# Performance work log

Measured on AMD Instinct MI355X. Metric: run time of the kernel, lower is better.

Reference implementation:

```python
import jax, jax.numpy as jnp
import numpy as np

N_REC = 12288  # 12 * nside^2, nside=32


def _mlp(x, w1, b1, w2, b2):
    # two-layer MLP with SiLU, as in GraphCast-style edge embedders
    return jnp.dot(jax.nn.silu(jnp.dot(x, w1) + b1), w2) + b2


def setup_inputs() -> dict:
    key = jax.random.key(0)
    ks = jax.random.split(key, 12)
    B, E, D_X, D_EDGE = 2, 393216, 128, 4
    EDGE_IN, EDGE_OUT, LIN_OUT = D_EDGE + D_X, 256, 256

    def glorot(k, shape):
        fan = shape[0] + shape[1]
        return jax.random.normal(k, shape, jnp.float32) * jnp.sqrt(2.0 / fan)

    return {
        "x": jax.random.normal(ks[0], (B, E, D_X), jnp.float32),
        "edge_attr": jax.random.normal(ks[1], (E, D_EDGE), jnp.float32),
        "edge_index": jax.random.randint(ks[2], (2, E), 0, N_REC, jnp.int64),
        "w1e": glorot(ks[3], (EDGE_IN, EDGE_OUT)),
        "b1e": jnp.zeros((EDGE_OUT,), jnp.float32),
        "w2e": glorot(ks[4], (EDGE_OUT, EDGE_OUT)),
        "b2e": jnp.zeros((EDGE_OUT,), jnp.float32),
        "w1f": glorot(ks[5], (EDGE_OUT, LIN_OUT)),
        "b1f": jnp.zeros((LIN_OUT,), jnp.float32),
        "w2f": glorot(ks[6], (LIN_OUT, LIN_OUT)),
        "b2f": jnp.zeros((LIN_OUT,), jnp.float32),
    }


def reference(x, edge_attr, edge_index, w1e, b1e, w2e, b2e, w1f, b1f, w2f, b2f):
    B = x.shape[0]
    # broadcast edge_attr over batch and concat with per-edge grid features
    ea = jnp.broadcast_to(edge_attr[None], (B,) + edge_attr.shape)  # [B,E,d_edge]
    v_g_prime = jnp.concatenate([ea, x], axis=-1)                    # [B,E,edge_in]
    v_g = _mlp(v_g_prime, w1e, b1e, w2e, b2e)                        # [B,E,edge_out]
    # scatter-sum edges into receiver nodes (edge_index[1]) along dim 1
    recv = edge_index[1]
    v_m_sum = jnp.zeros((B, N_REC, v_g.shape[-1]), v_g.dtype).at[:, recv].add(v_g)
    return _mlp(v_m_sum, w1f, b1f, w2f, b2f)                         # [B,N_REC,lin_out]
```

## Files before the change

### kernel.cpp

```cpp
#include <hip/hip_runtime.h>
#include <hip/hip_bf16.h>

#define E_EDGES 393216
#define NRECV   12288
#define DX      128
#define BATCH   2

typedef short bf16x8 __attribute__((ext_vector_type(8)));
typedef float f32x4  __attribute__((ext_vector_type(4)));

__device__ __forceinline__ unsigned short f2bf(float f) {
  union { float f; unsigned u; } v; v.f = f;
  unsigned r = v.u + 0x7FFFu + ((v.u >> 16) & 1u);
  return (unsigned short)(r >> 16);
}

__device__ __forceinline__ unsigned pk2(float a, float b) {
  __hip_bfloat162 h = __float22bfloat162_rn(make_float2(a, b));
  union { __hip_bfloat162 h; unsigned u; } c; c.h = h;
  return c.u;
}

__device__ __forceinline__ float silu_f(float v) {
  float e = __builtin_amdgcn_exp2f(v * -1.44269504089f);
  return v * __builtin_amdgcn_rcpf(1.0f + e);
}

__global__ __launch_bounds__(256) void zero_kernel(float4* __restrict__ p, int n4) {
  int i = blockIdx.x * 256 + threadIdx.x;
  int stride = gridDim.x * 256;
  float4 z = make_float4(0.f, 0.f, 0.f, 0.f);
  for (; i < n4; i += stride) p[i] = z;
}

__global__ __launch_bounds__(256) void swz_all_kernel(
    const float* __restrict__ w1e, const float* __restrict__ b1e,
    const float* __restrict__ w2e, const float* __restrict__ w1f,
    const float* __restrict__ w2f,
    unsigned short* __restrict__ w1sw, unsigned short* __restrict__ w2esw,
    unsigned short* __restrict__ w1fsw, unsigned short* __restrict__ w2fsw) {
  int blk = blockIdx.x;
  if (blk < 160) {
    int t = blk * 256 + threadIdx.x;
    int j = t & 7, l = (t >> 3) & 63, rest = t >> 9;
    int nf = rest & 15, ks = rest >> 4;
    int k = ks * 32 + (l >> 4) * 8 + j;
    int n = nf * 16 + (l & 15);
    float v = (k < 132) ? w1e[k * 256 + n] : (k == 132 ? b1e[n] : 0.0f);
    w1sw[t] = f2bf(v);
  } else {
    int g = blk - 160;
    int which = g >> 8;
    int t = (g & 255) * 256 + threadIdx.x;
    const float* W = (which == 0) ? w2e : (which == 1) ? w1f : w2f;
    unsigned short* O = (which == 0) ? w2esw : (which == 1) ? w1fsw : w2fsw;
    int j = t & 7, l = (t >> 3) & 63, rest = t >> 9;
    int nf = rest & 15, ks = rest >> 4;
    int k = ks * 32 + (l >> 4) * 8 + j;
    int n = nf * 16 + (l & 15);
    O[t] = f2bf(W[k * 256 + n]);
  }
}

__global__ void hist_kernel(const int* __restrict__ recv, int* __restrict__ cnt) {
  int e = blockIdx.x * 256 + threadIdx.x;
  if (e < E_EDGES) atomicAdd(&cnt[recv[e]], 1);
}

__global__ __launch_bounds__(256) void scan_kernel(const int* __restrict__ cnt,
                                                   int* __restrict__ head) {
  __shared__ int ts[256];
  const int t = threadIdx.x;
  const int base = t * 48;
  int s = 0;
#pragma unroll
  for (int i = 0; i < 48; ++i) s += cnt[base + i];
  ts[t] = s;
  __syncthreads();
  for (int d = 1; d < 256; d <<= 1) {
    int v = (t >= d) ? ts[t - d] : 0;
    __syncthreads();
    ts[t] += v;
    __syncthreads();
  }
  int run = (t == 0) ? 0 : ts[t - 1];
  for (int i = 0; i < 48; ++i) { head[base + i] = run; run += cnt[base + i]; }
}

__global__ void scatter_kernel(const int* __restrict__ recv, int* __restrict__ head,
                               int* __restrict__ perm) {
  int e = blockIdx.x * 256 + threadIdx.x;
  if (e < E_EDGES) {
    int pos = atomicAdd(&head[recv[e]], 1);
    perm[pos] = e;
  }
}

__global__ __launch_bounds__(256, 4) void edge_kernel(
    const float* __restrict__ x, const float* __restrict__ edge_attr,
    const int* __restrict__ recv, const int* __restrict__ perm,
    const unsigned short* __restrict__ w1sw, float* __restrict__ s) {
  __shared__ __align__(16) char As[64 * 384];
  __shared__ int rs[64];
  __shared__ int seg_recv[64];
  __shared__ unsigned seg32[16];

  const int tid = threadIdx.x;
  const int l  = tid & 63;
  const int w  = tid >> 6;
  const int lo = l & 15, hi = l >> 4;
  const int p0 = blockIdx.x * 64;
  const int b  = blockIdx.y;

  const int r = tid >> 2, q = tid & 3;
  const int er = perm[p0 + r];
  const float4* xr = (const float4*)(x + ((size_t)b * E_EDGES + er) * DX);
  float4 xv[8];
#pragma unroll
  for (int i = 0; i < 8; ++i) xv[i] = xr[i * 4 + q];

  float4 ea;
  if (tid < 64) {
    int e1 = perm[p0 + tid];
    rs[tid] = recv[e1];
    ea = *(const float4*)(edge_attr + (size_t)e1 * 4);
  }

  for (int idx = tid; idx < 960; idx += 256) {
    int rr = idx / 15, k2 = idx - rr * 15;
    int byte0 = 264 + 8 * k2;
    uint2 vz = make_uint2(k2 == 0 ? 0x00003F80u : 0u, 0u);
    *(uint2*)(As + rr * 384 + (byte0 ^ ((rr & 7) << 4))) = vz;
  }

  {
    const int rx = (r & 7) << 4;
#pragma unroll
    for (int i = 0; i < 8; ++i) {
      int t = i * 4 + q;
      int byte0 = 8 + 8 * t;
      *(uint2*)(As + r * 384 + (byte0 ^ rx)) =
          make_uint2(pk2(xv[i].x, xv[i].y), pk2(xv[i].z, xv[i].w));
    }
  }
  if (tid < 64) {
    *(uint2*)(As + tid * 384 + ((tid & 7) << 4)) =
        make_uint2(pk2(ea.x, ea.y), pk2(ea.z, ea.w));
  }
  __syncthreads();

  const int flag = (l == 63) || (rs[l + 1] != rs[l]);
  const unsigned long long segmask = __ballot(flag);
  const int nseg = __popcll(segmask);
  if (tid < 64) {
    int sid = __popcll(segmask & ((1ull << tid) - 1ull));
    ((unsigned char*)seg32)[tid] = (unsigned char)sid;
    if (flag) seg_recv[sid] = rs[tid];
  }

  f32x4 acc[4][4] = {};
  const int axor = (lo & 7) << 4;
#pragma unroll
  for (int kk = 0; kk < 5; ++kk) {
    bf16x8 a[4], bb[4];
#pragma unroll
    for (int mf = 0; mf < 4; ++mf)
      a[mf] = *(const bf16x8*)(As + (mf * 16 + lo) * 384 + ((kk * 64 + hi * 16) ^ axor));
#pragma unroll
    for (int nf = 0; nf < 4; ++nf)
      bb[nf] = *(const bf16x8*)&w1sw[(size_t)(((kk * 16) + (w * 4 + nf)) * 64 + l) * 8];
#pragma unroll
    for (int mf = 0; mf < 4; ++mf)
#pragma unroll
      for (int nf = 0; nf < 4; ++nf)
        acc[mf][nf] = __builtin_amdgcn_mfma_f32_16x16x32_bf16(a[mf], bb[nf], acc[mf][nf], 0, 0, 0);
  }
  __syncthreads();

  unsigned pkd[4][4][2];
#pragma unroll
  for (int mf = 0; mf < 4; ++mf)
#pragma unroll
    for (int nf = 0; nf < 4; ++nf) {
      float v0 = silu_f(acc[mf][nf][0]);
      float v1 = silu_f(acc[mf][nf][1]);
      float v2 = silu_f(acc[mf][nf][2]);
      float v3 = silu_f(acc[mf][nf][3]);
      pkd[mf][nf][0] = pk2(v0, v1);
      pkd[mf][nf][1] = pk2(v2, v3);
    }

  unsigned hbw[2][4][4];
#pragma unroll
  for (int kk = 0; kk < 2; ++kk)
#pragma unroll
    for (int nf = 0; nf < 4; ++nf)
#pragma unroll
      for (int t = 0; t < 4; ++t) {
        int src = ((hi & 1) * 2 + (t >> 1)) * 16 + lo;
        int a0 = __shfl((int)pkd[2 * kk][nf][t & 1], src, 64);
        int a1 = __shfl((int)pkd[2 * kk + 1][nf][t & 1], src, 64);
        hbw[kk][nf][t] = (hi & 2) ? (unsigned)a1 : (unsigned)a0;
      }

  float* sb = s + (size_t)b * NRECV * 256;
  for (int p = 0; p * 16 < nseg; ++p) {
    union { unsigned u[4]; bf16x8 v; } ia[2];
#pragma unroll
    for (int kk = 0; kk < 2; ++kk) {
      unsigned d0 = seg32[kk * 8 + hi * 2];
      unsigned d1 = seg32[kk * 8 + hi * 2 + 1];
      unsigned tgt = (unsigned)(lo + p * 16);
      ia[kk].u[0] = (((d0 & 255u) == tgt) ? 0x3F80u : 0u) |
                    ((((d0 >> 8) & 255u) == tgt) ? 0x3F800000u : 0u);
      ia[kk].u[1] = ((((d0 >> 16) & 255u) == tgt) ? 0x3F80u : 0u) |
                    (((d0 >> 24) == tgt) ? 0x3F800000u : 0u);
      ia[kk].u[2] = (((d1 & 255u) == tgt) ? 0x3F80u : 0u) |
                    ((((d1 >> 8) & 255u) == tgt) ? 0x3F800000u : 0u);
      ia[kk].u[3] = ((((d1 >> 16) & 255u) == tgt) ? 0x3F80u : 0u) |
                    (((d1 >> 24) == tgt) ? 0x3F800000u : 0u);
    }
    f32x4 accS[4] = {};
#pragma unroll
    for (int kk = 0; kk < 2; ++kk)
#pragma unroll
      for (int nf = 0; nf < 4; ++nf) {
        union { unsigned u[4]; bf16x8 v; } hb;
        hb.u[0] = hbw[kk][nf][0]; hb.u[1] = hbw[kk][nf][1];
        hb.u[2] = hbw[kk][nf][2]; hb.u[3] = hbw[kk][nf][3];
        accS[nf] = __builtin_amdgcn_mfma_f32_16x16x32_bf16(ia[kk].v, hb.v, accS[nf], 0, 0, 0);
      }
#pragma unroll
    for (int j = 0; j < 4; ++j) {
      int sidx = p * 16 + hi * 4 + j;
      if (sidx < nseg) {
        int rcv = seg_recv[sidx];
#pragma unroll
        for (int nf = 0; nf < 4; ++nf)
          atomicAdd(sb + (size_t)rcv * 256 + w * 64 + nf * 16 + lo, accS[nf][j]);
      }
    }
  }
}

__device__ __forceinline__ void gemm64(const unsigned short* Ns,
                                       const unsigned short* __restrict__ Bsw,
                                       int w, int l, f32x4 acc[4][4]) {
  const int lo = l & 15, hi = l >> 4;
#pragma unroll
  for (int kk = 0; kk < 8; ++kk) {
    bf16x8 a[4], bb[4];
#pragma unroll
    for (int mf = 0; mf < 4; ++mf)
      a[mf] = *(const bf16x8*)&Ns[(mf * 16 + lo) * 264 + kk * 32 + hi * 8];
#pragma unroll
    for (int nf = 0; nf < 4; ++nf)
      bb[nf] = *(const bf16x8*)&Bsw[(size_t)(((kk * 16) + (w * 4 + nf)) * 64 + l) * 8];
#pragma unroll
    for (int mf = 0; mf < 4; ++mf)
#pragma unroll
      for (int nf = 0; nf < 4; ++nf)
        acc[mf][nf] = __builtin_amdgcn_mfma_f32_16x16x32_bf16(a[mf], bb[nf], acc[mf][nf], 0, 0, 0);
  }
}

__global__ __launch_bounds__(256) void node_kernel(
    const float* __restrict__ s, const int* __restrict__ cnt,
    const unsigned short* __restrict__ w2esw, const float* __restrict__ b2e,
    const unsigned short* __restrict__ w1fsw, const float* __restrict__ b1f,
    const unsigned short* __restrict__ w2fsw, const float* __restrict__ b2f,
    float* __restrict__ out) {
  __shared__ unsigned short Ns[64 * 264];
  __shared__ int   cntl[64];
  __shared__ float bias1[256], bias2[256], bias3[256];

  const int tid = threadIdx.x;
  const int l  = tid & 63;
  const int w  = tid >> 6;
  const int lo = l & 15, hi = l >> 4;
  const int r0 = blockIdx.x * 64;
  const int b  = blockIdx.y;

  const float4* sb = (const float4*)(s + ((size_t)b * NRECV + r0) * 256);
#pragma unroll
  for (int i = 0; i < 16; ++i) {
    int f = i * 256 + tid;
    float4 v = sb[f];
    int g = f * 4;
    int row = g >> 8, col = g & 255;
    *(uint2*)&Ns[row * 264 + col] = make_uint2(pk2(v.x, v.y), pk2(v.z, v.w));
  }
  if (tid < 64) cntl[tid] = cnt[r0 + tid];
  bias1[tid] = b2e[tid];
  bias2[tid] = b1f[tid];
  bias3[tid] = b2f[tid];
  __syncthreads();

  {
    f32x4 acc[4][4] = {};
    gemm64(Ns, w2esw, w, l, acc);
    __syncthreads();
#pragma unroll
    for (int mf = 0; mf < 4; ++mf)
#pragma unroll
      for (int nf = 0; nf < 4; ++nf) {
        const int col = w * 64 + nf * 16 + lo;
#pragma unroll
        for (int j = 0; j < 4; ++j) {
          const int row = mf * 16 + hi * 4 + j;
          float v = acc[mf][nf][j] + (float)cntl[row] * bias1[col];
          Ns[row * 264 + col] = f2bf(v);
        }
      }
    __syncthreads();
  }
  {
    f32x4 acc[4][4] = {};
    gemm64(Ns, w1fsw, w, l, acc);
    __syncthreads();
#pragma unroll
    for (int mf = 0; mf < 4; ++mf)
#pragma unroll
      for (int nf = 0; nf < 4; ++nf) {
        const int col = w * 64 + nf * 16 + lo;
#pragma unroll
        for (int j = 0; j < 4; ++j) {
          const int row = mf * 16 + hi * 4 + j;
          float v = silu_f(acc[mf][nf][j] + bias2[col]);
          Ns[row * 264 + col] = f2bf(v);
        }
      }
    __syncthreads();
  }
  {
    f32x4 acc[4][4] = {};
    gemm64(Ns, w2fsw, w, l, acc);
#pragma unroll
    for (int mf = 0; mf < 4; ++mf)
#pragma unroll
      for (int nf = 0; nf < 4; ++nf) {
        const int col = w * 64 + nf * 16 + lo;
#pragma unroll
        for (int j = 0; j < 4; ++j) {
          const int row = mf * 16 + hi * 4 + j;
          out[((size_t)b * NRECV + r0 + row) * 256 + col] = acc[mf][nf][j] + bias3[col];
        }
      }
  }
}

extern "C" void kernel_launch(void* const* d_in, const int* in_sizes, int n_in,
                              void* d_out, int out_size, void* d_ws, size_t ws_size,
                              hipStream_t stream) {
  const float* x         = (const float*)d_in[0];
  const float* edge_attr = (const float*)d_in[1];
  const int*   edge_idx  = (const int*)d_in[2];
  const float* w1e       = (const float*)d_in[3];
  const float* b1e       = (const float*)d_in[4];
  const float* w2e       = (const float*)d_in[5];
  const float* b2e       = (const float*)d_in[6];
  const float* w1f       = (const float*)d_in[7];
  const float* b1f       = (const float*)d_in[8];
  const float* w2f       = (const float*)d_in[9];
  const float* b2f       = (const float*)d_in[10];
  float* out = (float*)d_out;

  char* ws = (char*)d_ws;
  float*          sbuf  = (float*)(ws + 0);
  int*            cnt   = (int*)(ws + 25165824);
  int*            head  = (int*)(ws + 25214976);
  int*            perm  = (int*)(ws + 25264128);
  unsigned short* w1sw  = (unsigned short*)(ws + 26836992);
  unsigned short* w2esw = (unsigned short*)(ws + 26918912);
  unsigned short* w1fsw = (unsigned short*)(ws + 27049984);
  unsigned short* w2fsw = (unsigned short*)(ws + 27181056);

  zero_kernel<<<2048, 256, 0, stream>>>((float4*)ws, 1575936);

  swz_all_kernel<<<928, 256, 0, stream>>>(w1e, b1e, w2e, w1f, w2f,
                                          w1sw, w2esw, w1fsw, w2fsw);

  const int* recv = edge_idx + E_EDGES;
  hist_kernel<<<E_EDGES / 256, 256, 0, stream>>>(recv, cnt);
  scan_kernel<<<1, 256, 0, stream>>>(cnt, head);
  scatter_kernel<<<E_EDGES / 256, 256, 0, stream>>>(recv, head, perm);

  dim3 eg(E_EDGES / 64, BATCH);
  edge_kernel<<<eg, 256, 0, stream>>>(x, edge_attr, recv, perm, w1sw, sbuf);

  dim3 ng(NRECV / 64, BATCH);
  node_kernel<<<ng, 256, 0, stream>>>(sbuf, cnt, w2esw, b2e, w1fsw, b1f, w2fsw, b2f, out);
}
```

Before: 250.3 us.

## Make edge kernel persistent over eight tiles with register double-buffered prefetch

Each edge_kernel block now handles 8 consecutive 64-edge tiles instead of one. While the current tile runs its GEMM and segment-reduce, the next tile's x rows, edge_attr and receiver ids are prefetched into a second register set. The zero padding of the shared A tile is written once per block rather than once per tile. The aim is to hide gather latency behind MFMA work and cut per-block launch overhead, at the cost of more registers, fewer blocks (768×2) and possibly lower occupancy.

```diff
diff --git a/kernel.cpp b/kernel.cpp
--- a/kernel.cpp
+++ b/kernel.cpp
@@ -5,6 +5,7 @@
 #define NRECV   12288
 #define DX      128
 #define BATCH   2
+#define NT      8
 
 typedef short bf16x8 __attribute__((ext_vector_type(8)));
 typedef float f32x4  __attribute__((ext_vector_type(4)));
@@ -109,22 +110,12 @@
   const int l  = tid & 63;
   const int w  = tid >> 6;
   const int lo = l & 15, hi = l >> 4;
-  const int p0 = blockIdx.x * 64;
+  const int tile0 = blockIdx.x * NT;
   const int b  = blockIdx.y;
-
   const int r = tid >> 2, q = tid & 3;
-  const int er = perm[p0 + r];
-  const float4* xr = (const float4*)(x + ((size_t)b * E_EDGES + er) * DX);
-  float4 xv[8];
-#pragma unroll
-  for (int i = 0; i < 8; ++i) xv[i] = xr[i * 4 + q];
-
-  float4 ea;
-  if (tid < 64) {
-    int e1 = perm[p0 + tid];
-    rs[tid] = recv[e1];
-    ea = *(const float4*)(edge_attr + (size_t)e1 * 4);
-  }
+  const int rx = (r & 7) << 4;
+  const int axor = (lo & 7) << 4;
+  float* const sb = s + (size_t)b * NRECV * 256;
 
   for (int idx = tid; idx < 960; idx += 256) {
     int rr = idx / 15, k2 = idx - rr * 15;
@@ -133,113 +124,140 @@
     *(uint2*)(As + rr * 384 + (byte0 ^ ((rr & 7) << 4))) = vz;
   }
 
+  float4 xvA[8], xvB[8];
+  float4 eaA = make_float4(0, 0, 0, 0), eaB = make_float4(0, 0, 0, 0);
+  int rsA = 0, rsB = 0;
+
   {
-    const int rx = (r & 7) << 4;
+    const int p0 = tile0 * 64;
+    const int er = perm[p0 + r];
+    const float4* xr = (const float4*)(x + ((size_t)b * E_EDGES + er) * DX);
+#pragma unroll
+    for (int i = 0; i < 8; ++i) xvA[i] = xr[i * 4 + q];
+    if (tid < 64) {
+      int e1 = perm[p0 + tid];
+      rsA = recv[e1];
+      eaA = *(const float4*)(edge_attr + (size_t)e1 * 4);
+    }
+  }
+
+  auto body = [&](int t, float4 (&xvC)[8], float4& eaC, int& rsC,
+                  float4 (&xvN)[8], float4& eaN, int& rsN) {
 #pragma unroll
     for (int i = 0; i < 8; ++i) {
-      int t = i * 4 + q;
-      int byte0 = 8 + 8 * t;
+      int t_ = i * 4 + q;
+      int byte0 = 8 + 8 * t_;
       *(uint2*)(As + r * 384 + (byte0 ^ rx)) =
-          make_uint2(pk2(xv[i].x, xv[i].y), pk2(xv[i].z, xv[i].w));
-    }
-  }
-  if (tid < 64) {
-    *(uint2*)(As + tid * 384 + ((tid & 7) << 4)) =
-        make_uint2(pk2(ea.x, ea.y), pk2(ea.z, ea.w));
-  }
-  __syncthreads();
-
-  const int flag = (l == 63) || (rs[l + 1] != rs[l]);
-  const unsigned long long segmask = __ballot(flag);
-  const int nseg = __popcll(segmask);
-  if (tid < 64) {
-    int sid = __popcll(segmask & ((1ull << tid) - 1ull));
-    ((unsigned char*)seg32)[tid] = (unsigned char)sid;
-    if (flag) seg_recv[sid] = rs[tid];
-  }
-
-  f32x4 acc[4][4] = {};
-  const int axor = (lo & 7) << 4;
-#pragma unroll
-  for (int kk = 0; kk < 5; ++kk) {
-    bf16x8 a[4], bb[4];
-#pragma unroll
-    for (int mf = 0; mf < 4; ++mf)
-      a[mf] = *(const bf16x8*)(As + (mf * 16 + lo) * 384 + ((kk * 64 + hi * 16) ^ axor));
-#pragma unroll
-    for (int nf = 0; nf < 4; ++nf)
-      bb[nf] = *(const bf16x8*)&w1sw[(size_t)(((kk * 16) + (w * 4 + nf)) * 64 + l) * 8];
-#pragma unroll
-    for (int mf = 0; mf < 4; ++mf)
-#pragma unroll
-      for (int nf = 0; nf < 4; ++nf)
-        acc[mf][nf] = __builtin_amdgcn_mfma_f32_16x16x32_bf16(a[mf], bb[nf], acc[mf][nf], 0, 0, 0);
-  }
-  __syncthreads();
-
-  unsigned pkd[4][4][2];
-#pragma unroll
-  for (int mf = 0; mf < 4; ++mf)
-#pragma unroll
-    for (int nf = 0; nf < 4; ++nf) {
-      float v0 = silu_f(acc[mf][nf][0]);
-      float v1 = silu_f(acc[mf][nf][1]);
-      float v2 = silu_f(acc[mf][nf][2]);
-      float v3 = silu_f(acc[mf][nf][3]);
-      pkd[mf][nf][0] = pk2(v0, v1);
-      pkd[mf][nf][1] = pk2(v2, v3);
-    }
-
-  unsigned hbw[2][4][4];
-#pragma unroll
-  for (int kk = 0; kk < 2; ++kk)
-#pragma unroll
-    for (int nf = 0; nf < 4; ++nf)
-#pragma unroll
-      for (int t = 0; t < 4; ++t) {
-        int src = ((hi & 1) * 2 + (t >> 1)) * 16 + lo;
-        int a0 = __shfl((int)pkd[2 * kk][nf][t & 1], src, 64);
-        int a1 = __shfl((int)pkd[2 * kk + 1][nf][t & 1], src, 64);
-        hbw[kk][nf][t] = (hi & 2) ? (unsigned)a1 : (unsigned)a0;
-      }
-
-  float* sb = s + (size_t)b * NRECV * 256;
-  for (int p = 0; p * 16 < nseg; ++p) {
-    union { unsigned u[4]; bf16x8 v; } ia[2];
-#pragma unroll
-    for (int kk = 0; kk < 2; ++kk) {
-      unsigned d0 = seg32[kk * 8 + hi * 2];
-      unsigned d1 = seg32[kk * 8 + hi * 2 + 1];
-      unsigned tgt = (unsigned)(lo + p * 16);
-      ia[kk].u[0] = (((d0 & 255u) == tgt) ? 0x3F80u : 0u) |
-                    ((((d0 >> 8) & 255u) == tgt) ? 0x3F800000u : 0u);
-      ia[kk].u[1] = ((((d0 >> 16) & 255u) == tgt) ? 0x3F80u : 0u) |
-                    (((d0 >> 24) == tgt) ? 0x3F800000u : 0u);
-      ia[kk].u[2] = (((d1 & 255u) == tgt) ? 0x3F80u : 0u) |
-                    ((((d1 >> 8) & 255u) == tgt) ? 0x3F800000u : 0u);
-      ia[kk].u[3] = ((((d1 >> 16) & 255u) == tgt) ? 0x3F80u : 0u) |
-                    (((d1 >> 24) == tgt) ? 0x3F800000u : 0u);
-    }
-    f32x4 accS[4] = {};
+          make_uint2(pk2(xvC[i].x, xvC[i].y), pk2(xvC[i].z, xvC[i].w));
+    }
+    if (tid < 64) {
+      *(uint2*)(As + tid * 384 + ((tid & 7) << 4)) =
+          make_uint2(pk2(eaC.x, eaC.y), pk2(eaC.z, eaC.w));
+      rs[tid] = rsC;
+    }
+    __syncthreads();
+
+    const int flag = (l == 63) || (rs[l + 1] != rs[l]);
+    const unsigned long long segmask = __ballot(flag);
+    const int nseg = __popcll(segmask);
+    if (tid < 64) {
+      int sid = __popcll(segmask & ((1ull << tid) - 1ull));
+      ((unsigned char*)seg32)[tid] = (unsigned char)sid;
+      if (flag) seg_recv[sid] = rsC;
+    }
+
+    if (t + 1 < NT) {
+      const int p0n = (tile0 + t + 1) * 64;
+      const int ern = perm[p0n + r];
+      const float4* xrn = (const float4*)(x + ((size_t)b * E_EDGES + ern) * DX);
+#pragma unroll
+      for (int i = 0; i < 8; ++i) xvN[i] = xrn[i * 4 + q];
+      if (tid < 64) {
+        int e1 = perm[p0n + tid];
+        rsN = recv[e1];
+        eaN = *(const float4*)(edge_attr + (size_t)e1 * 4);
+      }
+    }
+
+    f32x4 acc[4][4] = {};
+#pragma unroll
+    for (int kk = 0; kk < 5; ++kk) {
+      bf16x8 a[4];
+#pragma unroll
+      for (int mf = 0; mf < 4; ++mf)
+        a[mf] = *(const bf16x8*)(As + (mf * 16 + lo) * 384 + ((kk * 64 + hi * 16) ^ axor));
+#pragma unroll
+      for (int nf = 0; nf < 4; ++nf) {
+        bf16x8 bb = *(const bf16x8*)&w1sw[(size_t)(((kk * 16) + (w * 4 + nf)) * 64 + l) * 8];
+#pragma unroll
+        for (int mf = 0; mf < 4; ++mf)
+          acc[mf][nf] = __builtin_amdgcn_mfma_f32_16x16x32_bf16(a[mf], bb, acc[mf][nf], 0, 0, 0);
+      }
+    }
+    __syncthreads();
+
+    unsigned hbw[2][4][4];
 #pragma unroll
     for (int kk = 0; kk < 2; ++kk)
 #pragma unroll
       for (int nf = 0; nf < 4; ++nf) {
-        union { unsigned u[4]; bf16x8 v; } hb;
-        hb.u[0] = hbw[kk][nf][0]; hb.u[1] = hbw[kk][nf][1];
-        hb.u[2] = hbw[kk][nf][2]; hb.u[3] = hbw[kk][nf][3];
-        accS[nf] = __builtin_amdgcn_mfma_f32_16x16x32_bf16(ia[kk].v, hb.v, accS[nf], 0, 0, 0);
-      }
-#pragma unroll
-    for (int j = 0; j < 4; ++j) {
-      int sidx = p * 16 + hi * 4 + j;
-      if (sidx < nseg) {
-        int rcv = seg_recv[sidx];
-#pragma unroll
-        for (int nf = 0; nf < 4; ++nf)
-          atomicAdd(sb + (size_t)rcv * 256 + w * 64 + nf * 16 + lo, accS[nf][j]);
-      }
-    }
+        unsigned pA[2], pB[2];
+        pA[0] = pk2(silu_f(acc[2 * kk][nf][0]), silu_f(acc[2 * kk][nf][1]));
+        pA[1] = pk2(silu_f(acc[2 * kk][nf][2]), silu_f(acc[2 * kk][nf][3]));
+        pB[0] = pk2(silu_f(acc[2 * kk + 1][nf][0]), silu_f(acc[2 * kk + 1][nf][1]));
+        pB[1] = pk2(silu_f(acc[2 * kk + 1][nf][2]), silu_f(acc[2 * kk + 1][nf][3]));
+#pragma unroll
+        for (int t4 = 0; t4 < 4; ++t4) {
+          int src = ((hi & 1) * 2 + (t4 >> 1)) * 16 + lo;
+          int a0 = __shfl((int)pA[t4 & 1], src, 64);
+          int a1 = __shfl((int)pB[t4 & 1], src, 64);
+          hbw[kk][nf][t4] = (hi & 2) ? (unsigned)a1 : (unsigned)a0;
+        }
+      }
+
+    for (int p = 0; p * 16 < nseg; ++p) {
+      union { unsigned u[4]; bf16x8 v; } ia[2];
+#pragma unroll
+      for (int kk = 0; kk < 2; ++kk) {
+        unsigned d0 = seg32[kk * 8 + hi * 2];
+        unsigned d1 = seg32[kk * 8 + hi * 2 + 1];
+        unsigned tgt = (unsigned)(lo + p * 16);
+        ia[kk].u[0] = (((d0 & 255u) == tgt) ? 0x3F80u : 0u) |
+                      ((((d0 >> 8) & 255u) == tgt) ? 0x3F800000u : 0u);
+        ia[kk].u[1] = ((((d0 >> 16) & 255u) == tgt) ? 0x3F80u : 0u) |
+                      (((d0 >> 24) == tgt) ? 0x3F800000u : 0u);
+        ia[kk].u[2] = (((d1 & 255u) == tgt) ? 0x3F80u : 0u) |
+                      ((((d1 >> 8) & 255u) == tgt) ? 0x3F800000u : 0u);
+        ia[kk].u[3] = ((((d1 >> 16) & 255u) == tgt) ? 0x3F80u : 0u) |
+                      (((d1 >> 24) == tgt) ? 0x3F800000u : 0u);
+      }
+      f32x4 accS[4] = {};
+#pragma unroll
+      for (int kk = 0; kk < 2; ++kk)
+#pragma unroll
+        for (int nf = 0; nf < 4; ++nf) {
+          union { unsigned u[4]; bf16x8 v; } hb;
+          hb.u[0] = hbw[kk][nf][0]; hb.u[1] = hbw[kk][nf][1];
+          hb.u[2] = hbw[kk][nf][2]; hb.u[3] = hbw[kk][nf][3];
+          accS[nf] = __builtin_amdgcn_mfma_f32_16x16x32_bf16(ia[kk].v, hb.v, accS[nf], 0, 0, 0);
+        }
+#pragma unroll
+      for (int j = 0; j < 4; ++j) {
+        int sidx = p * 16 + hi * 4 + j;
+        if (sidx < nseg) {
+          int rcv = seg_recv[sidx];
+#pragma unroll
+          for (int nf = 0; nf < 4; ++nf)
+            atomicAdd(sb + (size_t)rcv * 256 + w * 64 + nf * 16 + lo, accS[nf][j]);
+        }
+      }
+    }
+  };
+
+#pragma unroll 1
+  for (int tt = 0; tt < NT; tt += 2) {
+    body(tt, xvA, eaA, rsA, xvB, eaB, rsB);
+    body(tt + 1, xvB, eaB, rsB, xvA, eaA, rsA);
   }
 }
 
@@ -385,7 +403,7 @@
   scan_kernel<<<1, 256, 0, stream>>>(cnt, head);
   scatter_kernel<<<E_EDGES / 256, 256, 0, stream>>>(recv, head, perm);
 
-  dim3 eg(E_EDGES / 64, BATCH);
+  dim3 eg(E_EDGES / (64 * NT), BATCH);
   edge_kernel<<<eg, 256, 0, stream>>>(x, edge_attr, recv, perm, w1sw, sbuf);
 
   dim3 ng(NRECV / 64, BATCH);
```

Result: slower. 649.7 us (+159.6%).
